# Kernel tuning notes

Measured on AMD Instinct MI355X. Metric: run time of the kernel, lower is better.

## Reference

```python
import jax, jax.numpy as jnp
import numpy as np

EPS = 1e-8  # torch.nn.CosineSimilarity eps


def setup_inputs() -> dict:
    key = jax.random.key(0)
    k1, k2, k3 = jax.random.split(key, 3)
    C, S, D = 1024, 16, 512
    x = jax.random.normal(k1, (C, S, D), dtype=jnp.float32)
    w = jax.random.normal(k2, (1,), dtype=jnp.float32)
    b = jax.random.normal(k3, (1,), dtype=jnp.float32)
    return {"x": x, "w": w, "b": b}


def reference(x, w, b):
    # stable_ge2e: leave-one-out positive centroids, full negative centroids.
    C, S, D = x.shape
    wp = jax.nn.softplus(w)  # (1,)

    sum_c = x.sum(axis=1)                      # (C, D)
    mean_c = sum_c / S                         # negative centroids (C, D)
    loo = (sum_c[:, None, :] - x) / (S - 1.0)  # leave-one-out centroids (C, S, D)

    nx = jnp.linalg.norm(x, axis=-1)           # (C, S)
    nmean = jnp.linalg.norm(mean_c, axis=-1)   # (C,)
    nloo = jnp.linalg.norm(loo, axis=-1)       # (C, S)

    # cosine similarities (clamped denominator, as in torch CosineSimilarity)
    sim_neg = jnp.einsum('jid,kd->jik', x, mean_c) / jnp.maximum(
        nx[:, :, None] * nmean[None, None, :], EPS)          # (C, S, C)
    sim_pos = jnp.einsum('jid,jid->ji', x, loo) / jnp.maximum(nx * nloo, EPS)  # (C, S)

    # on the diagonal k == j use the leave-one-out positive centroid
    eye = jnp.eye(C, dtype=bool)
    sim = jnp.where(eye[:, None, :], sim_pos[:, :, None], sim_neg)  # (C, S, C)

    logits = wp * sim + b
    logS = jax.nn.log_softmax(logits, axis=-1)
    Sji_j = jnp.einsum('jij->ji', logS)                        # (C, S) diagonal
    Sji_k = jax.scipy.special.logsumexp(logS, axis=-1)         # (C, S) (== 0 post-softmax)
    loss = -(Sji_j - Sji_k).reshape(-1)
    return loss.mean()
```

## Files before the change

### kernel.cpp

```cpp
#include <hip/hip_runtime.h>
#include <math.h>

#define CC 1024
#define SS 16
#define DD 512
#define RR (CC*SS)
#define EPSV 1e-8f
#define LDB 520
#define CHUNK 32

typedef __attribute__((ext_vector_type(8))) short short8;
typedef __attribute__((ext_vector_type(4))) float f32x4;
typedef unsigned short ushort_t;

__device__ __forceinline__ unsigned short f2bf(float f) {
  unsigned u = __float_as_uint(f);
  u += 0x7fffu + ((u >> 16) & 1u);
  return (unsigned short)(u >> 16);
}

__device__ __forceinline__ void async16(void* l, const void* g) {
  __builtin_amdgcn_global_load_lds(
      (const __attribute__((address_space(1))) void*)g,
      (__attribute__((address_space(3))) void*)l, 16, 0, 0);
}

__device__ __forceinline__ float softplusf(float v) {
  return (v > 20.f) ? v : log1pf(expf(v));
}

__global__ __launch_bounds__(256) void k_pre(
    const float* __restrict__ x, ushort_t* __restrict__ mn,
    float* __restrict__ nx, float* __restrict__ simpos,
    ushort_t* __restrict__ xn) {
  __shared__ float xs[SS * DD];
  __shared__ float sums[DD];
  __shared__ float red[4];
  __shared__ float snm;
  __shared__ float rinv[SS];
  const int j = blockIdx.x, tid = threadIdx.x;
  const int wid = tid >> 6, lane = tid & 63;
  const float4* xj = (const float4*)(x + (size_t)j * SS * DD);
  float4* xs4 = (float4*)xs;
#pragma unroll
  for (int t = 0; t < 8; ++t) xs4[tid + t * 256] = xj[tid + t * 256];
  __syncthreads();

  float sx = 0.f, sy = 0.f;
  const float2* xs2 = (const float2*)xs;
#pragma unroll
  for (int i = 0; i < SS; ++i) {
    float2 v = xs2[i * (DD / 2) + tid];
    sx += v.x; sy += v.y;
  }
  ((float2*)sums)[tid] = make_float2(sx, sy);
  const float mxs = sx * (1.0f / SS), mys = sy * (1.0f / SS);
  float m2 = mxs * mxs + mys * mys;
#pragma unroll
  for (int off = 32; off > 0; off >>= 1) m2 += __shfl_xor(m2, off, 64);
  if (lane == 0) red[wid] = m2;
  __syncthreads();
  if (tid == 0) snm = sqrtf(red[0] + red[1] + red[2] + red[3]);
  __syncthreads();
  const float inm = (1.0f / SS) / snm;
  {
    unsigned lo = f2bf(sx * inm), hi = f2bf(sy * inm);
    ((unsigned*)(mn + (size_t)j * DD))[tid] = lo | (hi << 16);
  }

  for (int i = wid; i < SS; i += 4) {
    float nx2 = 0.f, dxs = 0.f, t2 = 0.f;
    const float2* xr2 = (const float2*)(xs + i * DD);
    const float2* sm2 = (const float2*)sums;
#pragma unroll
    for (int d2 = 0; d2 < DD / 2; d2 += 64) {
      float2 xv = xr2[d2 + lane];
      float2 sc = sm2[d2 + lane];
      nx2 = fmaf(xv.x, xv.x, fmaf(xv.y, xv.y, nx2));
      dxs = fmaf(xv.x, sc.x, fmaf(xv.y, sc.y, dxs));
      float tx = sc.x - xv.x, ty = sc.y - xv.y;
      t2 = fmaf(tx, tx, fmaf(ty, ty, t2));
    }
#pragma unroll
    for (int off = 32; off > 0; off >>= 1) {
      nx2 += __shfl_xor(nx2, off, 64);
      dxs += __shfl_xor(dxs, off, 64);
      t2  += __shfl_xor(t2,  off, 64);
    }
    if (lane == 0) {
      float nxv = sqrtf(nx2);
      float tn  = sqrtf(t2);
      float num = (dxs - nx2) * (1.0f / (SS - 1));
      float den = fmaxf(nxv * tn * (1.0f / (SS - 1)), EPSV);
      nx[j * SS + i] = nxv;
      rinv[i] = 1.0f / nxv;
      simpos[j * SS + i] = num / den;
    }
  }
  __syncthreads();
  if (xn) {
    uint2* dst = (uint2*)(xn + (size_t)j * SS * DD);
    const float4* src4 = (const float4*)xs;
#pragma unroll
    for (int t = 0; t < 8; ++t) {
      const int idx = tid + t * 256;
      const float ri = rinv[idx >> 7];
      float4 v = src4[idx];
      uint2 o;
      o.x = (unsigned)f2bf(v.x * ri) | ((unsigned)f2bf(v.y * ri) << 16);
      o.y = (unsigned)f2bf(v.z * ri) | ((unsigned)f2bf(v.w * ri) << 16);
      dst[idx] = o;
    }
  }
}

template <bool USE_XN>
__global__ __launch_bounds__(128, 1) void k_gemm(
    const float* __restrict__ x, const ushort_t* __restrict__ xn,
    const ushort_t* __restrict__ mn, const float* __restrict__ nx,
    const float* __restrict__ simpos, const float* __restrict__ wptr,
    const float* __restrict__ bptr, float* __restrict__ ps) {
  __shared__ ushort_t bs[2][CHUNK * LDB];
  const int tid = threadIdx.x;
  const int wid = tid >> 6, lane = tid & 63;
  const int cL = lane & 15, quad = lane >> 4;
  const int bid = (int)blockIdx.x;
  const int rb = bid & 255, cb = bid >> 8;
  const int r0 = rb * 64, cbase = cb * 512;
  const float wp = softplusf(wptr[0]), bv = bptr[0];
  const int row0w = r0 + wid * 32;

  short8 af[2][16];
  int jw[2];
  float sp[2][4], sacc[2][4];
#pragma unroll
  for (int rt = 0; rt < 2; ++rt) {
    const int row = row0w + rt * 16 + cL;
    if (USE_XN) {
      const short8* src = (const short8*)(xn + (size_t)row * DD);
#pragma unroll
      for (int kc = 0; kc < 16; ++kc) af[rt][kc] = src[kc * 4 + quad];
    } else {
      const float* xr = x + (size_t)row * DD;
      const float invn = 1.0f / nx[row];
#pragma unroll
      for (int kc = 0; kc < 16; ++kc) {
        const int k0 = kc * 32 + quad * 8;
        float4 p = *(const float4*)(xr + k0);
        float4 q = *(const float4*)(xr + k0 + 4);
        short8 v;
        v[0] = f2bf(p.x * invn); v[1] = f2bf(p.y * invn);
        v[2] = f2bf(p.z * invn); v[3] = f2bf(p.w * invn);
        v[4] = f2bf(q.x * invn); v[5] = f2bf(q.y * invn);
        v[6] = f2bf(q.z * invn); v[7] = f2bf(q.w * invn);
        af[rt][kc] = v;
      }
    }
    jw[rt] = (row0w + rt * 16) >> 4;
#pragma unroll
    for (int r = 0; r < 4; ++r) {
      sp[rt][r] = simpos[row0w + rt * 16 + quad * 4 + r];
      sacc[rt][r] = 0.f;
    }
  }

  {
    const ushort_t* gsrc = mn + (size_t)cbase * DD;
#pragma unroll
    for (int t = 0; t < 16; ++t) {
      const int rr = wid + t * 2;
      async16(&bs[0][rr * LDB + lane * 8], gsrc + (size_t)rr * DD + lane * 8);
    }
  }
  __syncthreads();

  for (int cc = 0; cc < 16; ++cc) {
    if (cc < 15) {
      const ushort_t* gsrc = mn + (size_t)(cbase + (cc + 1) * CHUNK) * DD;
      ushort_t* dst = bs[(cc + 1) & 1];
#pragma unroll
      for (int t = 0; t < 16; ++t) {
        const int rr = wid + t * 2;
        async16(&dst[rr * LDB + lane * 8], gsrc + (size_t)rr * DD + lane * 8);
      }
    }
    const ushort_t* B = bs[cc & 1];
    f32x4 acc[2][2];
#pragma unroll
    for (int rt = 0; rt < 2; ++rt)
#pragma unroll
      for (int f = 0; f < 2; ++f) acc[rt][f] = (f32x4){0.f, 0.f, 0.f, 0.f};
#pragma unroll
    for (int kc = 0; kc < 16; ++kc) {
      short8 bfr[2];
#pragma unroll
      for (int f = 0; f < 2; ++f)
        bfr[f] = *(const short8*)&B[(f * 16 + cL) * LDB + kc * 32 + quad * 8];
#pragma unroll
      for (int rt = 0; rt < 2; ++rt)
#pragma unroll
        for (int f = 0; f < 2; ++f)
          acc[rt][f] = __builtin_amdgcn_mfma_f32_16x16x32_bf16(
              af[rt][kc], bfr[f], acc[rt][f], 0, 0, 0);
    }
    const int c0 = cbase + cc * CHUNK;
#pragma unroll
    for (int rt = 0; rt < 2; ++rt)
#pragma unroll
      for (int f = 0; f < 2; ++f) {
        const int cg = c0 + f * 16 + cL;
        const bool diag = (cg == jw[rt]);
#pragma unroll
        for (int r = 0; r < 4; ++r) {
          const float sim = diag ? sp[rt][r] : acc[rt][f][r];
          sacc[rt][r] += __expf(fmaf(wp, sim, bv));
        }
      }
    __syncthreads();
  }

#pragma unroll
  for (int rt = 0; rt < 2; ++rt)
#pragma unroll
    for (int r = 0; r < 4; ++r) {
      float v = sacc[rt][r];
#pragma unroll
      for (int off = 1; off < 16; off <<= 1) v += __shfl_xor(v, off, 64);
      if (cL == 0)
        ps[(size_t)(row0w + rt * 16 + quad * 4 + r) * 2 + cb] = v;
    }
}

__global__ __launch_bounds__(1024) void k_loss(
    const float* __restrict__ ps, const float* __restrict__ simpos,
    const float* __restrict__ wptr, const float* __restrict__ bptr,
    float* __restrict__ out) {
  __shared__ float red[16];
  const int tid = threadIdx.x;
  const float wp = softplusf(wptr[0]), bv = bptr[0];
  float acc = 0.f;
#pragma unroll
  for (int i = 0; i < RR / 1024; ++i) {
    const int row = i * 1024 + tid;
    const float2 v = ((const float2*)ps)[row];
    acc += logf(v.x + v.y) - fmaf(wp, simpos[row], bv);
  }
#pragma unroll
  for (int off = 32; off > 0; off >>= 1) acc += __shfl_xor(acc, off, 64);
  if ((tid & 63) == 0) red[tid >> 6] = acc;
  __syncthreads();
  if (tid < 64) {
    float v = (tid < 16) ? red[tid] : 0.f;
#pragma unroll
    for (int off = 8; off > 0; off >>= 1) v += __shfl_xor(v, off, 64);
    if (tid == 0) out[0] = v * (1.0f / RR);
  }
}

extern "C" void kernel_launch(void* const* d_in, const int* in_sizes, int n_in,
                              void* d_out, int out_size, void* d_ws, size_t ws_size,
                              hipStream_t stream) {
  const float* x = (const float*)d_in[0];
  const float* w = (const float*)d_in[1];
  const float* b = (const float*)d_in[2];
  float* out = (float*)d_out;

  const size_t xn_bytes = (size_t)RR * DD * 2;
  const size_t rest = (size_t)CC * DD * 2 + (size_t)RR * 4 * 2 +
                      (size_t)RR * 2 * 4;
  const bool use_xn = ws_size >= xn_bytes + rest + 256;

  char* base = (char*)d_ws;
  ushort_t* xn = use_xn ? (ushort_t*)base : nullptr;
  char* p = base + (use_xn ? xn_bytes : 0);
  ushort_t* mn = (ushort_t*)p;  p += (size_t)CC * DD * 2;
  float* nx     = (float*)p;    p += (size_t)RR * 4;
  float* simpos = (float*)p;    p += (size_t)RR * 4;
  float* ps     = (float*)p;

  k_pre<<<CC, 256, 0, stream>>>(x, mn, nx, simpos, xn);
  if (use_xn)
    k_gemm<true><<<512, 128, 0, stream>>>(x, xn, mn, nx, simpos, w, b, ps);
  else
    k_gemm<false><<<512, 128, 0, stream>>>(x, xn, mn, nx, simpos, w, b, ps);
  k_loss<<<1, 1024, 0, stream>>>(ps, simpos, w, b, out);
}
```

Measured before the change: 115.1 us.

## Overlap B-tile prefetch with MFMA using explicit vmcnt waits and raw barriers

```diff
diff --git a/kernel.cpp b/kernel.cpp
--- a/kernel.cpp
+++ b/kernel.cpp
@@ -8,6 +8,7 @@
 #define EPSV 1e-8f
 #define LDB 520
 #define CHUNK 32
+#define NCHUNK 16
 
 typedef __attribute__((ext_vector_type(8))) short short8;
 typedef __attribute__((ext_vector_type(4))) float f32x4;
@@ -28,6 +29,9 @@
 __device__ __forceinline__ float softplusf(float v) {
   return (v > 20.f) ? v : log1pf(expf(v));
 }
+
+#define SBAR()   __builtin_amdgcn_s_barrier()
+#define SCHED0() __builtin_amdgcn_sched_barrier(0)
 
 __global__ __launch_bounds__(256) void k_pre(
     const float* __restrict__ x, ushort_t* __restrict__ mn,
@@ -68,33 +72,34 @@
     ((unsigned*)(mn + (size_t)j * DD))[tid] = lo | (hi << 16);
   }
 
-  for (int i = wid; i < SS; i += 4) {
+  {
+    const int g = tid >> 4, l16 = tid & 15;
     float nx2 = 0.f, dxs = 0.f, t2 = 0.f;
-    const float2* xr2 = (const float2*)(xs + i * DD);
+    const float2* xr2 = (const float2*)(xs + g * DD);
     const float2* sm2 = (const float2*)sums;
 #pragma unroll
-    for (int d2 = 0; d2 < DD / 2; d2 += 64) {
-      float2 xv = xr2[d2 + lane];
-      float2 sc = sm2[d2 + lane];
+    for (int t = 0; t < 16; ++t) {
+      float2 xv = xr2[l16 + t * 16];
+      float2 sc = sm2[l16 + t * 16];
       nx2 = fmaf(xv.x, xv.x, fmaf(xv.y, xv.y, nx2));
       dxs = fmaf(xv.x, sc.x, fmaf(xv.y, sc.y, dxs));
       float tx = sc.x - xv.x, ty = sc.y - xv.y;
       t2 = fmaf(tx, tx, fmaf(ty, ty, t2));
     }
 #pragma unroll
-    for (int off = 32; off > 0; off >>= 1) {
+    for (int off = 1; off < 16; off <<= 1) {
       nx2 += __shfl_xor(nx2, off, 64);
       dxs += __shfl_xor(dxs, off, 64);
       t2  += __shfl_xor(t2,  off, 64);
     }
-    if (lane == 0) {
+    if (l16 == 0) {
       float nxv = sqrtf(nx2);
       float tn  = sqrtf(t2);
       float num = (dxs - nx2) * (1.0f / (SS - 1));
       float den = fmaxf(nxv * tn * (1.0f / (SS - 1)), EPSV);
-      nx[j * SS + i] = nxv;
-      rinv[i] = 1.0f / nxv;
-      simpos[j * SS + i] = num / den;
+      nx[j * SS + g] = nxv;
+      rinv[g] = 1.0f / nxv;
+      simpos[j * SS + g] = num / den;
     }
   }
   __syncthreads();
@@ -115,7 +120,7 @@
 }
 
 template <bool USE_XN>
-__global__ __launch_bounds__(128, 1) void k_gemm(
+__global__ __launch_bounds__(128, 2) void k_gemm(
     const float* __restrict__ x, const ushort_t* __restrict__ xn,
     const ushort_t* __restrict__ mn, const float* __restrict__ nx,
     const float* __restrict__ simpos, const float* __restrict__ wptr,
@@ -172,10 +177,10 @@
       async16(&bs[0][rr * LDB + lane * 8], gsrc + (size_t)rr * DD + lane * 8);
     }
   }
-  __syncthreads();
-
-  for (int cc = 0; cc < 16; ++cc) {
-    if (cc < 15) {
+
+#pragma unroll
+  for (int cc = 0; cc < NCHUNK; ++cc) {
+    if (cc < NCHUNK - 1) {
       const ushort_t* gsrc = mn + (size_t)(cbase + (cc + 1) * CHUNK) * DD;
       ushort_t* dst = bs[(cc + 1) & 1];
 #pragma unroll
@@ -183,7 +188,15 @@
         const int rr = wid + t * 2;
         async16(&dst[rr * LDB + lane * 8], gsrc + (size_t)rr * DD + lane * 8);
       }
-    }
+      SCHED0();
+      asm volatile("s_waitcnt vmcnt(16)" ::: "memory");
+    } else {
+      asm volatile("s_waitcnt vmcnt(0)" ::: "memory");
+    }
+    SCHED0();
+    SBAR();
+    SCHED0();
+
     const ushort_t* B = bs[cc & 1];
     f32x4 acc[2][2];
 #pragma unroll
@@ -216,7 +229,11 @@
           sacc[rt][r] += __expf(fmaf(wp, sim, bv));
         }
       }
-    __syncthreads();
+    if (cc < NCHUNK - 1) {
+      SCHED0();
+      SBAR();
+      SCHED0();
+    }
   }
 
 #pragma unroll
```

Result: no change. 113.2 us (-1.6%).
